# Kernel optimization log

Hardware: AMD Instinct MI355X
Metric: run time of the kernel (lower is better)

Reference implementation:

```python
import jax, jax.numpy as jnp
import numpy as np
from jax import lax

N, CIN, H, W = 4, 1024, 56, 56
CB = 256          # bottleneck channels
K = 9             # 3x3 kernel taps


def _conv(x, w, b, stride=1, padding='SAME'):
    y = lax.conv_general_dilated(x, w, (stride, stride), padding,
                                 dimension_numbers=('NCHW', 'OIHW', 'NCHW'))
    return y + b[None, :, None, None]


def _bilinear_gather(feat, ys, xs):
    # feat: [N,C,H,W]; ys, xs: [N,P] float sample coords. Zero padding outside.
    n, c, h, w = feat.shape
    y0 = jnp.floor(ys); x0 = jnp.floor(xs)
    wy1 = ys - y0; wy0 = 1.0 - wy1
    wx1 = xs - x0; wx0 = 1.0 - wx1
    flat = feat.reshape(n, c, h * w)

    def g(yi, xi):
        valid = (yi >= 0) & (yi <= h - 1) & (xi >= 0) & (xi <= w - 1)
        yc = jnp.clip(yi, 0, h - 1).astype(jnp.int32)
        xc = jnp.clip(xi, 0, w - 1).astype(jnp.int32)
        idx = (yc * w + xc)  # [N,P]
        vals = jnp.take_along_axis(flat, idx[:, None, :], axis=2)  # [N,C,P]
        return vals * valid[:, None, :].astype(feat.dtype)

    out = (g(y0, x0) * (wy0 * wx0)[:, None, :]
           + g(y0, x0 + 1) * (wy0 * wx1)[:, None, :]
           + g(y0 + 1, x0) * (wy1 * wx0)[:, None, :]
           + g(y0 + 1, x0 + 1) * (wy1 * wx1)[:, None, :])
    return out  # [N,C,P]


def _deform_conv3x3(feat, w, b, w_off, b_off):
    # DCNv1: offsets predicted by a standard 3x3 conv (18 = 2*K channels),
    # then bilinear-sample input at p + p_k + offset, accumulate with kernel w.
    n, c, h, ww = feat.shape
    off = _conv(feat, w_off, b_off)                 # [N, 2K, H, W]
    off = off.reshape(n, K, 2, h, ww)
    dy, dx = off[:, :, 0], off[:, :, 1]             # [N,K,H,W]
    ki, kj = jnp.meshgrid(jnp.arange(3), jnp.arange(3), indexing='ij')
    ky = (ki.reshape(-1) - 1).astype(feat.dtype)    # kernel dy offsets, rate=1
    kx = (kj.reshape(-1) - 1).astype(feat.dtype)
    hh = jnp.arange(h, dtype=feat.dtype)
    wc = jnp.arange(ww, dtype=feat.dtype)
    ys = hh[None, None, :, None] + ky[None, :, None, None] + dy   # [N,K,H,W]
    xs = wc[None, None, None, :] + kx[None, :, None, None] + dx
    sampled = _bilinear_gather(feat, ys.reshape(n, -1), xs.reshape(n, -1))
    sampled = sampled.reshape(n, c, K, h, ww)       # [N,C,K,H,W]
    out = jnp.einsum('nckhw,ock->nohw', sampled, w.reshape(w.shape[0], c, K))
    return out + b[None, :, None, None]


def setup_inputs() -> dict:
    key = jax.random.key(0)
    ks = jax.random.split(key, 6)
    x = jax.random.normal(ks[0], (N, CIN, H, W), dtype=jnp.float32)
    w1 = jax.random.normal(ks[1], (CB, CIN, 1, 1), dtype=jnp.float32) * 0.02
    b1 = jnp.zeros((CB,), jnp.float32)
    w_off = jax.random.normal(ks[2], (2 * K, CB, 3, 3), dtype=jnp.float32) * 0.01
    b_off = jnp.zeros((2 * K,), jnp.float32)
    w2 = jax.random.normal(ks[3], (CB, CB, 3, 3), dtype=jnp.float32) * 0.02
    b2 = jnp.zeros((CB,), jnp.float32)
    w3 = jax.random.normal(ks[4], (CIN, CB, 1, 1), dtype=jnp.float32) * 0.02
    b3 = jnp.zeros((CIN,), jnp.float32)
    return {"x": x, "w1": w1, "b1": b1, "w_off": w_off, "b_off": b_off,
            "w2": w2, "b2": b2, "w3": w3, "b3": b3}


def reference(x, w1, b1, w_off, b_off, w2, b2, w3, b3):
    # shortcut is identity (in_channels == out_channels, stride=1)
    r = jax.nn.relu(_conv(x, w1, b1))                      # conv1 1x1 + relu
    r = jax.nn.relu(_deform_conv3x3(r, w2, b2, w_off, b_off))  # deform 3x3 + relu
    r = _conv(r, w3, b3)                                   # conv3 1x1, no act
    return jax.nn.relu(x + r)
```

## Files before the change

### kernel.cpp

```cpp
#include <hip/hip_runtime.h>
#include <hip/hip_bf16.h>

#define N_   4
#define CIN  1024
#define H_   56
#define W_   56
#define HW   3136
#define CB   256
#define KK   9
#define OFFC 18

typedef __attribute__((ext_vector_type(8))) short short8;
typedef __attribute__((ext_vector_type(4))) short short4v;
typedef __attribute__((ext_vector_type(4))) float float4v;
typedef unsigned short ushort_t;

__device__ inline ushort_t bf16_rne(float f) {
    unsigned int u = __float_as_uint(f);
    unsigned int r = (u + 0x7FFFu + ((u >> 16) & 1u)) >> 16;
    return (ushort_t)r;
}
__device__ inline void split_bf16(float f, ushort_t& hi, ushort_t& lo) {
    ushort_t h = bf16_rne(f);
    float hf = __uint_as_float(((unsigned int)h) << 16);
    hi = h;
    lo = bf16_rne(f - hf);
}
__device__ inline short8 ld_frag_lds(const ushort_t* base) {
    short4v a = *(const short4v*)base;
    short4v b = *(const short4v*)(base + 4);
    return __builtin_shufflevector(a, b, 0, 1, 2, 3, 4, 5, 6, 7);
}
__device__ inline void lds_barrier() {
    asm volatile("s_waitcnt lgkmcnt(0)" ::: "memory");
    __builtin_amdgcn_s_barrier();
    __builtin_amdgcn_sched_barrier(0);
}

__global__ void __launch_bounds__(256) pack_weights_kernel(
    const float* __restrict__ w1, const float* __restrict__ w2,
    const float* __restrict__ w3, const float* __restrict__ w_off,
    ushort_t* __restrict__ w1p, ushort_t* __restrict__ w2p,
    ushort_t* __restrict__ w3p, ushort_t* __restrict__ wofp)
{
    int e = blockIdx.x * 256 + threadIdx.x;
    if (e < 256 * 1024) {
        int o = e >> 10, k = e & 1023;
        ushort_t hi, lo; split_bf16(w1[e], hi, lo);
        w1p[(size_t)(o * 2 + 0) * 1024 + k] = hi;
        w1p[(size_t)(o * 2 + 1) * 1024 + k] = lo;
        return;
    }
    e -= 256 * 1024;
    if (e < 256 * 256 * 9) {
        int o = e / 2304; int rem = e % 2304; int c = rem / 9; int k = rem % 9;
        w2p[(size_t)(k * 256 + o) * 256 + c] = bf16_rne(w2[e]);
        return;
    }
    e -= 256 * 256 * 9;
    if (e < 1024 * 256) {
        int o = e >> 8, k = e & 255;
        ushort_t hi, lo; split_bf16(w3[e], hi, lo);
        w3p[(size_t)(o * 2 + 0) * 256 + k] = hi;
        w3p[(size_t)(o * 2 + 1) * 256 + k] = lo;
        return;
    }
    e -= 1024 * 256;
    if (e < 9 * 32 * 256) {
        int k = e / (32 * 256);
        int rem = e % (32 * 256);
        int m = rem >> 8, c = rem & 255;
        float v = (m < OFFC) ? w_off[((size_t)m * 256 + c) * 9 + k] : 0.f;
        wofp[e] = bf16_rne(v);
    }
}

template <int MFRAG, bool RELU, bool RESID>
__global__ void __launch_bounds__(256, 4) conv1x1_mfma_kernel(
    const ushort_t* __restrict__ Wp,
    const float* __restrict__ Xin,
    const float* __restrict__ bias,
    const float* __restrict__ resid,
    float* __restrict__ Cout,
    int M, int Kdim)
{
    __shared__ ushort_t Bs[64][36];

    const int tid  = threadIdx.x;
    const int wave = tid >> 6;
    const int lane = tid & 63;
    const int l15  = lane & 15;
    const int quad = lane >> 4;
    const int pBase = blockIdx.x * 64;
    const int mBase = blockIdx.y * (MFRAG * 64) + wave * (MFRAG * 16);
    const int n     = blockIdx.z;
    const float* Xn = Xin + (size_t)n * Kdim * HW;

    float4v acc[MFRAG][4];
#pragma unroll
    for (int i = 0; i < MFRAG; ++i)
#pragma unroll
        for (int j = 0; j < 4; ++j) acc[i][j] = (float4v)(0.f);

    const int kk = tid >> 3;
    const int pq = (tid & 7) * 8;

    for (int k0 = 0; k0 < Kdim; k0 += 32) {
        const float* src = &Xn[(size_t)(k0 + kk) * HW + pBase + pq];
        float4 v0 = *reinterpret_cast<const float4*>(src);
        float4 v1 = *reinterpret_cast<const float4*>(src + 4);
        __syncthreads();
        float vs[8] = {v0.x, v0.y, v0.z, v0.w, v1.x, v1.y, v1.z, v1.w};
#pragma unroll
        for (int j = 0; j < 8; ++j) Bs[pq + j][kk] = bf16_rne(vs[j]);
        __syncthreads();

        short8 ah[MFRAG], al[MFRAG];
#pragma unroll
        for (int mt = 0; mt < MFRAG; ++mt) {
            const ushort_t* arow = Wp +
                ((size_t)(mBase + mt * 16 + l15) * 2) * Kdim + k0 + quad * 8;
            ah[mt] = *(const short8*)(arow);
            al[mt] = *(const short8*)(arow + Kdim);
        }
        short8 bh[4];
#pragma unroll
        for (int nt = 0; nt < 4; ++nt)
            bh[nt] = ld_frag_lds(&Bs[nt * 16 + l15][quad * 8]);
#pragma unroll
        for (int mt = 0; mt < MFRAG; ++mt)
#pragma unroll
            for (int nt = 0; nt < 4; ++nt) {
                acc[mt][nt] = __builtin_amdgcn_mfma_f32_16x16x32_bf16(
                    ah[mt], bh[nt], acc[mt][nt], 0, 0, 0);
                acc[mt][nt] = __builtin_amdgcn_mfma_f32_16x16x32_bf16(
                    al[mt], bh[nt], acc[mt][nt], 0, 0, 0);
            }
    }

#pragma unroll
    for (int mt = 0; mt < MFRAG; ++mt)
#pragma unroll
        for (int rr = 0; rr < 4; ++rr) {
            int row = mBase + mt * 16 + quad * 4 + rr;
            float bv = bias[row];
#pragma unroll
            for (int nt = 0; nt < 4; ++nt) {
                int col = pBase + nt * 16 + l15;
                size_t idx = ((size_t)n * M + row) * HW + col;
                float v = acc[mt][nt][rr] + bv;
                if (RESID) v += resid[idx];
                if (RELU)  v = fmaxf(v, 0.f);
                Cout[idx] = v;
            }
        }
}

__global__ void __launch_bounds__(256, 2) offset_mfma_kernel(
    const float* __restrict__ r,
    const ushort_t* __restrict__ wofp,
    const float* __restrict__ b_off,
    float* __restrict__ off)
{
    __shared__ float win[32][174];

    const int tid  = threadIdx.x;
    const int h    = blockIdx.x;
    const int n    = blockIdx.y;
    const int wave = tid >> 6;
    const int lane = tid & 63;
    const int l15  = lane & 15;
    const int quad = lane >> 4;
    const float* rn = r + (size_t)n * CB * HW;

    const int p = wave * 16 + l15;

    float4v acc[2];
    acc[0] = (float4v)(0.f);
    acc[1] = (float4v)(0.f);

    for (int cb = 0; cb < CB; cb += 32) {
        __syncthreads();
        for (int f = tid; f < 32 * 3 * 14; f += 256) {
            int c = f / 42, remf = f % 42, row = remf / 14, x4 = (remf % 14) * 4;
            int yg = h - 1 + row;
            float4 v = {0.f, 0.f, 0.f, 0.f};
            if (yg >= 0 && yg < H_)
                v = *reinterpret_cast<const float4*>(
                    &rn[(size_t)(cb + c) * HW + yg * W_ + x4]);
            *reinterpret_cast<float4*>(&win[c][row * 56 + x4]) = v;
        }
        __syncthreads();

#pragma unroll
        for (int k = 0; k < KK; ++k) {
            const int ky = k / 3;
            const int dx = (k % 3) - 1;
            int x = p + dx;
            bool pvalid = (p < 56) && (x >= 0) && (x < 56);
            int xc = min(max(x, 0), 55);
            short8 bh;
#pragma unroll
            for (int j = 0; j < 8; ++j) {
                float v = win[quad * 8 + j][ky * 56 + xc];
                bh[j] = (short)bf16_rne(pvalid ? v : 0.f);
            }
#pragma unroll
            for (int mt = 0; mt < 2; ++mt) {
                const ushort_t* arow = wofp +
                    (size_t)(k * 32 + mt * 16 + l15) * 256 + cb + quad * 8;
                short8 ah = *(const short8*)arow;
                acc[mt] = __builtin_amdgcn_mfma_f32_16x16x32_bf16(
                    ah, bh, acc[mt], 0, 0, 0);
            }
        }
    }

    if (p < 56) {
#pragma unroll
        for (int mt = 0; mt < 2; ++mt)
#pragma unroll
            for (int rr = 0; rr < 4; ++rr) {
                int m = mt * 16 + quad * 4 + rr;
                if (m < OFFC)
                    off[((size_t)n * OFFC + m) * HW + h * W_ + p] =
                        acc[mt][rr] + b_off[m];
            }
    }
}

#define TPX   28
#define WROWS 5
#define WCOLS 36
#define WPOS  (WROWS * WCOLS)
#define CSTR  33
#define WITEMS (32 * WROWS * 9)
#define DBLK  (H_ * 2 * N_)

__global__ void __launch_bounds__(512, 2) deform_mfma_kernel(
    const float* __restrict__ r,
    const float* __restrict__ off,
    const ushort_t* __restrict__ w2p,
    const float* __restrict__ b2,
    float* __restrict__ r2)
{
    __shared__ float    win[WPOS][CSTR];
    __shared__ ushort_t Bs[KK][32][36];

    const int tid = threadIdx.x;
    const int bid = blockIdx.x;
    const int swz = (bid & 7) * (DBLK >> 3) + (bid >> 3);
    const int xh  = swz & 1;
    const int h   = (swz >> 1) % H_;
    const int n   = swz / (H_ * 2);
    const int xb  = xh * TPX;
    const float* rn   = r + (size_t)n * CB * HW;
    const float* offn = off + (size_t)n * OFFC * HW;

    int   bi0 = 0, bi1 = 0, bi2 = 0, bi3 = 0;
    float bw0 = 0.f, bw1 = 0.f, bw2 = 0.f, bw3 = 0.f;
    int   go0 = 0, go1 = 0, go2 = 0, go3 = 0;
    bool  bfast = true;
    const bool bactive = (tid < 288);
    const int  bk = bactive ? (tid / 32) : 0;
    const int  bp = bactive ? (tid % 32) : 0;
    if (bactive && bp < TPX) {
        int pg = xb + bp;
        float dy = offn[(size_t)(2 * bk) * HW + h * W_ + pg];
        float dx = offn[(size_t)(2 * bk + 1) * HW + h * W_ + pg];
        float ys = (float)(h + (bk / 3) - 1) + dy;
        float xs = (float)(pg + (bk % 3) - 1) + dx;
        float y0f = floorf(ys), x0f = floorf(xs);
        int y0 = (int)y0f, x0 = (int)x0f;
        float wy1 = ys - y0f, wy0 = 1.f - wy1;
        float wx1 = xs - x0f, wx0 = 1.f - wx1;
        int   wid[4]; float wg[4]; int gof[4]; bool fast = true;
#pragma unroll
        for (int u = 0; u < 2; ++u)
#pragma unroll
            for (int vv = 0; vv < 2; ++vv) {
                int yy = y0 + u, xx = x0 + vv;
                bool valid = (yy >= 0) && (yy <= 55) && (xx >= 0) && (xx <= 55);
                float wgt = valid ? (u ? wy1 : wy0) * (vv ? wx1 : wx0) : 0.f;
                int ry = yy - (h - 2);
                int rx = xx - (xb - 4);
                if (wgt != 0.f &&
                    (ry < 0 || ry >= WROWS || rx < 0 || rx >= WCOLS))
                    fast = false;
                int idx = min(max(ry, 0), WROWS - 1) * WCOLS +
                          min(max(rx, 0), WCOLS - 1);
                wid[u * 2 + vv] = idx;
                wg[u * 2 + vv]  = wgt;
                gof[u * 2 + vv] = valid ? (yy * W_ + xx) : 0;
            }
        bfast = fast;
        bi0 = wid[0]; bi1 = wid[1]; bi2 = wid[2]; bi3 = wid[3];
        bw0 = wg[0];  bw1 = wg[1];  bw2 = wg[2];  bw3 = wg[3];
        go0 = gof[0]; go1 = gof[1]; go2 = gof[2]; go3 = gof[3];
    }

    const int wave = tid >> 6;
    const int lane = tid & 63;
    const int l15  = lane & 15;
    const int quad = lane >> 4;
    const int mW   = wave * 32;

    float4v acc[2][2];
#pragma unroll
    for (int i = 0; i < 2; ++i)
#pragma unroll
        for (int j = 0; j < 2; ++j) acc[i][j] = (float4v)(0.f);

    auto wload = [&](int f, int cbg) -> float4 {
        int c = f / 45, remf = f % 45, row = remf / 9, q = remf % 9;
        int yg = min(max(h - 2 + row, 0), H_ - 1);
        int xg = xb - 4 + q * 4;
        const float* src = &rn[(size_t)(cbg + c) * HW + yg * W_];
        float4 v;
        if (xg >= 0 && xg <= W_ - 4) {
            v = *reinterpret_cast<const float4*>(src + xg);
        } else {
            v.x = src[min(max(xg + 0, 0), W_ - 1)];
            v.y = src[min(max(xg + 1, 0), W_ - 1)];
            v.z = src[min(max(xg + 2, 0), W_ - 1)];
            v.w = src[min(max(xg + 3, 0), W_ - 1)];
        }
        return v;
    };

    float4 pre[3];
#pragma unroll
    for (int i = 0; i < 3; ++i) {
        int f = tid + 512 * i;
        if (f < WITEMS) pre[i] = wload(f, 0);
    }

    for (int cb = 0; cb < CB; cb += 32) {
#pragma unroll
        for (int i = 0; i < 3; ++i) {
            int f = tid + 512 * i;
            if (f < WITEMS) {
                int c = f / 45, remf = f % 45, row = remf / 9, q = remf % 9;
                int pos = row * WCOLS + q * 4;
                float4 v = pre[i];
                win[pos + 0][c] = v.x;
                win[pos + 1][c] = v.y;
                win[pos + 2][c] = v.z;
                win[pos + 3][c] = v.w;
            }
        }
        if (cb + 32 < CB) {
#pragma unroll
            for (int i = 0; i < 3; ++i) {
                int f = tid + 512 * i;
                if (f < WITEMS) pre[i] = wload(f, cb + 32);
            }
        }
        lds_barrier();

        if (bactive) {
#pragma unroll
            for (int c4 = 0; c4 < 32; c4 += 4) {
                float s[4];
                if (bfast) {
#pragma unroll
                    for (int j = 0; j < 4; ++j) {
                        int c = c4 + j;
                        s[j] = bw0 * win[bi0][c] + bw1 * win[bi1][c] +
                               bw2 * win[bi2][c] + bw3 * win[bi3][c];
                    }
                } else {
#pragma unroll
                    for (int j = 0; j < 4; ++j) {
                        const float* rc = rn + (size_t)(cb + c4 + j) * HW;
                        s[j] = bw0 * rc[go0] + bw1 * rc[go1] +
                               bw2 * rc[go2] + bw3 * rc[go3];
                    }
                }
                short4v pk;
#pragma unroll
                for (int j = 0; j < 4; ++j) pk[j] = (short)bf16_rne(s[j]);
                *(short4v*)&Bs[bk][bp][c4] = pk;
            }
        }
        lds_barrier();

        __builtin_amdgcn_s_setprio(1);
#pragma unroll
        for (int k = 0; k < KK; ++k) {
            short8 ah[2];
#pragma unroll
            for (int mt = 0; mt < 2; ++mt) {
                const ushort_t* arow = w2p +
                    (size_t)(k * 256 + (mW + mt * 16 + l15)) * 256 +
                    cb + quad * 8;
                ah[mt] = *(const short8*)(arow);
            }
            short8 bh[2];
#pragma unroll
            for (int nt = 0; nt < 2; ++nt)
                bh[nt] = ld_frag_lds(&Bs[k][nt * 16 + l15][quad * 8]);
#pragma unroll
            for (int mt = 0; mt < 2; ++mt)
#pragma unroll
                for (int nt = 0; nt < 2; ++nt)
                    acc[mt][nt] = __builtin_amdgcn_mfma_f32_16x16x32_bf16(
                        ah[mt], bh[nt], acc[mt][nt], 0, 0, 0);
        }
        __builtin_amdgcn_s_setprio(0);
    }

#pragma unroll
    for (int mt = 0; mt < 2; ++mt)
#pragma unroll
        for (int rr = 0; rr < 4; ++rr) {
            int o = mW + mt * 16 + quad * 4 + rr;
            float bv = b2[o];
#pragma unroll
            for (int nt = 0; nt < 2; ++nt) {
                int p = nt * 16 + l15;
                if (p < TPX) {
                    float v = fmaxf(acc[mt][nt][rr] + bv, 0.f);
                    r2[((size_t)n * CB + o) * HW + h * W_ + xb + p] = v;
                }
            }
        }
}

extern "C" void kernel_launch(void* const* d_in, const int* in_sizes, int n_in,
                              void* d_out, int out_size, void* d_ws, size_t ws_size,
                              hipStream_t stream)
{
    const float* x     = (const float*)d_in[0];
    const float* w1    = (const float*)d_in[1];
    const float* b1    = (const float*)d_in[2];
    const float* w_off = (const float*)d_in[3];
    const float* b_off = (const float*)d_in[4];
    const float* w2    = (const float*)d_in[5];
    const float* b2    = (const float*)d_in[6];
    const float* w3    = (const float*)d_in[7];
    const float* b3    = (const float*)d_in[8];
    float* out = (float*)d_out;

    float* ws  = (float*)d_ws;
    float* r    = ws;
    float* r2   = r  + (size_t)N_ * CB * HW;
    float* offb = r2 + (size_t)N_ * CB * HW;
    ushort_t* w1p  = (ushort_t*)(offb + (size_t)N_ * OFFC * HW);
    ushort_t* w2p  = w1p + (size_t)256 * 2 * 1024;
    ushort_t* w3p  = w2p + (size_t)9 * 256 * 256;
    ushort_t* wofp = w3p + (size_t)1024 * 2 * 256;

    {
        int total = 256 * 1024 + 256 * 256 * 9 + 1024 * 256 + 9 * 32 * 256;
        pack_weights_kernel<<<(total + 255) / 256, 256, 0, stream>>>(
            w1, w2, w3, w_off, w1p, w2p, w3p, wofp);
    }
    {
        dim3 grid(HW / 64, CB / 128, N_);
        conv1x1_mfma_kernel<2, true, false><<<grid, 256, 0, stream>>>(
            w1p, x, b1, nullptr, r, CB, CIN);
    }
    {
        dim3 grid(H_, N_);
        offset_mfma_kernel<<<grid, 256, 0, stream>>>(r, wofp, b_off, offb);
    }
    {
        deform_mfma_kernel<<<DBLK, 512, 0, stream>>>(r, offb, w2p, b2, r2);
    }
    {
        dim3 grid(HW / 64, CIN / 128, N_);
        conv1x1_mfma_kernel<2, true, true><<<grid, 256, 0, stream>>>(
            w3p, r2, b3, x, out, CIN, CB);
    }
}
```

Before: 363.5 us.

## Shrink deform tile to 14 pixels per block with 256 threads and vectorized LDS gathers

The deformable conv kernel now processes 14 output pixels per block (four blocks per row) with 256 threads, where each wave covers 64 output channels against a single 16-pixel N tile. The goal is to double the number of blocks for better occupancy and load balance and to vectorize the bilinear gather with float4 LDS reads (channel stride padded to 36). Window stores are rotated across lanes to reduce bank conflicts. In exchange, the A-matrix weight fragments are reloaded from global memory by twice as many blocks, and a 16-wide MFMA tile with only 14 valid pixels wastes some MFMA work.

Result: slower. 527.9 us (+45.2%).

```diff
diff --git a/kernel.cpp b/kernel.cpp
--- a/kernel.cpp
+++ b/kernel.cpp
@@ -229,31 +229,31 @@
     }
 }
 
-#define TPX   28
+#define TPX   14
 #define WROWS 5
-#define WCOLS 36
+#define WCOLS 24
 #define WPOS  (WROWS * WCOLS)
-#define CSTR  33
-#define WITEMS (32 * WROWS * 9)
-#define DBLK  (H_ * 2 * N_)
-
-__global__ void __launch_bounds__(512, 2) deform_mfma_kernel(
+#define CSTR  36
+#define SITEMS (32 * WROWS * 6)
+#define DBLK  (H_ * 4 * N_)
+
+__global__ void __launch_bounds__(256, 4) deform_mfma_kernel(
     const float* __restrict__ r,
     const float* __restrict__ off,
     const ushort_t* __restrict__ w2p,
     const float* __restrict__ b2,
     float* __restrict__ r2)
 {
-    __shared__ float    win[WPOS][CSTR];
-    __shared__ ushort_t Bs[KK][32][36];
+    __shared__ __align__(16) float    win[WPOS][CSTR];
+    __shared__ __align__(16) ushort_t Bs[KK][16][36];
 
     const int tid = threadIdx.x;
     const int bid = blockIdx.x;
     const int swz = (bid & 7) * (DBLK >> 3) + (bid >> 3);
-    const int xh  = swz & 1;
-    const int h   = (swz >> 1) % H_;
-    const int n   = swz / (H_ * 2);
-    const int xb  = xh * TPX;
+    const int xq  = swz & 3;
+    const int h   = (swz >> 2) % H_;
+    const int n   = swz / (H_ * 4);
+    const int xb  = xq * TPX;
     const float* rn   = r + (size_t)n * CB * HW;
     const float* offn = off + (size_t)n * OFFC * HW;
 
@@ -261,9 +261,9 @@
     float bw0 = 0.f, bw1 = 0.f, bw2 = 0.f, bw3 = 0.f;
     int   go0 = 0, go1 = 0, go2 = 0, go3 = 0;
     bool  bfast = true;
-    const bool bactive = (tid < 288);
-    const int  bk = bactive ? (tid / 32) : 0;
-    const int  bp = bactive ? (tid % 32) : 0;
+    const bool bactive = (tid < KK * 16);
+    const int  bk = tid >> 4;
+    const int  bp = tid & 15;
     if (bactive && bp < TPX) {
         int pg = xb + bp;
         float dy = offn[(size_t)(2 * bk) * HW + h * W_ + pg];
@@ -303,16 +303,14 @@
     const int lane = tid & 63;
     const int l15  = lane & 15;
     const int quad = lane >> 4;
-    const int mW   = wave * 32;
-
-    float4v acc[2][2];
-#pragma unroll
-    for (int i = 0; i < 2; ++i)
-#pragma unroll
-        for (int j = 0; j < 2; ++j) acc[i][j] = (float4v)(0.f);
+    const int mW   = wave * 64;
+
+    float4v acc[4];
+#pragma unroll
+    for (int i = 0; i < 4; ++i) acc[i] = (float4v)(0.f);
 
     auto wload = [&](int f, int cbg) -> float4 {
-        int c = f / 45, remf = f % 45, row = remf / 9, q = remf % 9;
+        int c = f / 30, rem = f % 30, row = rem / 6, q = rem % 6;
         int yg = min(max(h - 2 + row, 0), H_ - 1);
         int xg = xb - 4 + q * 4;
         const float* src = &rn[(size_t)(cbg + c) * HW + yg * W_];
@@ -328,32 +326,35 @@
         return v;
     };
 
-    float4 pre[3];
-#pragma unroll
-    for (int i = 0; i < 3; ++i) {
-        int f = tid + 512 * i;
-        if (f < WITEMS) pre[i] = wload(f, 0);
+    float4 pre[4];
+#pragma unroll
+    for (int i = 0; i < 4; ++i) {
+        int f = tid + 256 * i;
+        if (f < SITEMS) pre[i] = wload(f, 0);
     }
 
     for (int cb = 0; cb < CB; cb += 32) {
 #pragma unroll
-        for (int i = 0; i < 3; ++i) {
-            int f = tid + 512 * i;
-            if (f < WITEMS) {
-                int c = f / 45, remf = f % 45, row = remf / 9, q = remf % 9;
+        for (int i = 0; i < 4; ++i) {
+            int f = tid + 256 * i;
+            if (f < SITEMS) {
+                int c = f / 30, rem = f % 30, row = rem / 6, q = rem % 6;
                 int pos = row * WCOLS + q * 4;
                 float4 v = pre[i];
-                win[pos + 0][c] = v.x;
-                win[pos + 1][c] = v.y;
-                win[pos + 2][c] = v.z;
-                win[pos + 3][c] = v.w;
+#pragma unroll
+                for (int t = 0; t < 4; ++t) {
+                    int j = (t + tid) & 3;
+                    float vj = (j == 0) ? v.x : (j == 1) ? v.y
+                             : (j == 2) ? v.z : v.w;
+                    win[pos + j][c] = vj;
+                }
             }
         }
         if (cb + 32 < CB) {
 #pragma unroll
-            for (int i = 0; i < 3; ++i) {
-                int f = tid + 512 * i;
-                if (f < WITEMS) pre[i] = wload(f, cb + 32);
+            for (int i = 0; i < 4; ++i) {
+                int f = tid + 256 * i;
+                if (f < SITEMS) pre[i] = wload(f, cb + 32);
             }
         }
         lds_barrier();
@@ -361,14 +362,13 @@
         if (bactive) {
 #pragma unroll
             for (int c4 = 0; c4 < 32; c4 += 4) {
-                float s[4];
+                float4v s;
                 if (bfast) {
-#pragma unroll
-                    for (int j = 0; j < 4; ++j) {
-                        int c = c4 + j;
-                        s[j] = bw0 * win[bi0][c] + bw1 * win[bi1][c] +
-                               bw2 * win[bi2][c] + bw3 * win[bi3][c];
-                    }
+                    float4v v0 = *(const float4v*)&win[bi0][c4];
+                    float4v v1 = *(const float4v*)&win[bi1][c4];
+                    float4v v2 = *(const float4v*)&win[bi2][c4];
+                    float4v v3 = *(const float4v*)&win[bi3][c4];
+                    s = bw0 * v0 + bw1 * v1 + bw2 * v2 + bw3 * v3;
                 } else {
 #pragma unroll
                     for (int j = 0; j < 4; ++j) {
@@ -388,43 +388,35 @@
         __builtin_amdgcn_s_setprio(1);
 #pragma unroll
         for (int k = 0; k < KK; ++k) {
-            short8 ah[2];
-#pragma unroll
-            for (int mt = 0; mt < 2; ++mt) {
+            short8 ah[4];
+#pragma unroll
+            for (int mt = 0; mt < 4; ++mt) {
                 const ushort_t* arow = w2p +
                     (size_t)(k * 256 + (mW + mt * 16 + l15)) * 256 +
                     cb + quad * 8;
                 ah[mt] = *(const short8*)(arow);
             }
-            short8 bh[2];
-#pragma unroll
-            for (int nt = 0; nt < 2; ++nt)
-                bh[nt] = ld_frag_lds(&Bs[k][nt * 16 + l15][quad * 8]);
-#pragma unroll
-            for (int mt = 0; mt < 2; ++mt)
-#pragma unroll
-                for (int nt = 0; nt < 2; ++nt)
-                    acc[mt][nt] = __builtin_amdgcn_mfma_f32_16x16x32_bf16(
-                        ah[mt], bh[nt], acc[mt][nt], 0, 0, 0);
+            short8 bh = ld_frag_lds(&Bs[k][l15][quad * 8]);
+#pragma unroll
+            for (int mt = 0; mt < 4; ++mt)
+                acc[mt] = __builtin_amdgcn_mfma_f32_16x16x32_bf16(
+                    ah[mt], bh, acc[mt], 0, 0, 0);
         }
         __builtin_amdgcn_s_setprio(0);
     }
 
-#pragma unroll
-    for (int mt = 0; mt < 2; ++mt)
-#pragma unroll
-        for (int rr = 0; rr < 4; ++rr) {
-            int o = mW + mt * 16 + quad * 4 + rr;
-            float bv = b2[o];
-#pragma unroll
-            for (int nt = 0; nt < 2; ++nt) {
-                int p = nt * 16 + l15;
-                if (p < TPX) {
-                    float v = fmaxf(acc[mt][nt][rr] + bv, 0.f);
-                    r2[((size_t)n * CB + o) * HW + h * W_ + xb + p] = v;
-                }
-            }
-        }
+    const int p = l15;
+    if (p < TPX) {
+        float* dst = r2 + (size_t)n * CB * HW + (size_t)h * W_ + xb + p;
+#pragma unroll
+        for (int mt = 0; mt < 4; ++mt)
+#pragma unroll
+            for (int rr = 0; rr < 4; ++rr) {
+                int o = mW + mt * 16 + quad * 4 + rr;
+                float v = fmaxf(acc[mt][rr] + b2[o], 0.f);
+                dst[(size_t)o * HW] = v;
+            }
+    }
 }
 
 extern "C" void kernel_launch(void* const* d_in, const int* in_sizes, int n_in,
@@ -466,7 +458,7 @@
         offset_mfma_kernel<<<grid, 256, 0, stream>>>(r, wofp, b_off, offb);
     }
     {
-        deform_mfma_kernel<<<DBLK, 512, 0, stream>>>(r, offb, w2p, b2, r2);
+        deform_mfma_kernel<<<DBLK, 256, 0, stream>>>(r, offb, w2p, b2, r2);
     }
     {
         dim3 grid(HW / 64, CIN / 128, N_);
```
